# Kernel tuning notes

Measured on AMD Instinct MI355X. Metric: run time of the kernel, lower is better.

## Reference

```python
import jax, jax.numpy as jnp
import numpy as np

EMBED_DIM = 768
NUM_HEADS = 12
HEAD_DIM = EMBED_DIM // NUM_HEADS
SCALE = HEAD_DIM ** -0.5


def setup_inputs() -> dict:
    key = jax.random.key(0)
    k1, k2, k3, k4, k5 = jax.random.split(key, 5)
    B, T = 8, 1024
    init = 0.02
    return {
        "hidden_states": jax.random.normal(k1, (B, T, EMBED_DIM), dtype=jnp.float32),
        "qkv_w": jax.random.normal(k2, (EMBED_DIM, 3 * EMBED_DIM), dtype=jnp.float32) * init,
        "qkv_b": jnp.zeros((3 * EMBED_DIM,), dtype=jnp.float32),
        "proj_w": jax.random.normal(k3, (EMBED_DIM, EMBED_DIM), dtype=jnp.float32) * init,
        "proj_b": jnp.zeros((EMBED_DIM,), dtype=jnp.float32),
    }


def reference(hidden_states, qkv_w, qkv_b, proj_w, proj_b):
    B, T, E = hidden_states.shape
    # fused QKV projection: [B, T, 3E] -> [3, B, H, T, Dh]
    mixed = hidden_states @ qkv_w + qkv_b
    mixed = mixed.reshape(B, T, 3, NUM_HEADS, HEAD_DIM).transpose(2, 0, 3, 1, 4)
    q, k, v = mixed[0], mixed[1], mixed[2]
    # scores: [B, H, T, T]
    scores = jnp.einsum("bhqd,bhkd->bhqk", q, k) * SCALE
    probs = jax.nn.softmax(scores, axis=-1)
    # context: [B, T, H, Dh] -> [B, T, E]
    ctx = jnp.einsum("bhqk,bhkd->bqhd", probs, v).reshape(B, T, E)
    return ctx @ proj_w + proj_b
```

## Files before the change

kernel.cpp:

```cpp
#include <hip/hip_runtime.h>
#include <hip/hip_bf16.h>

#define B_ 8
#define T_ 1024
#define E_ 768
#define H_ 12
#define DH_ 64
#define E3_ 2304
#define M_ (B_ * T_)
#define SCALE_LOG2E 0.18033688011112042f

typedef __attribute__((ext_vector_type(8))) short short8;
typedef __attribute__((ext_vector_type(4))) float float4_;
typedef __attribute__((ext_vector_type(4))) unsigned short ushort4_;

__device__ __forceinline__ unsigned short f2bf(float f) {
    union { float f; unsigned int u; } v; v.f = f;
    unsigned int r = v.u + 0x7fffu + ((v.u >> 16) & 1u);
    return (unsigned short)(r >> 16);
}

__device__ __forceinline__ void gld_lds16(const unsigned short* g, unsigned short* l) {
    __builtin_amdgcn_global_load_lds(
        (const __attribute__((address_space(1))) void*)g,
        (__attribute__((address_space(3))) void*)l,
        16, 0, 0);
}

__global__ __launch_bounds__(256) void prep(const float* __restrict__ hs,
                                            const float* __restrict__ qkv_w,
                                            const float* __restrict__ proj_w,
                                            unsigned short* __restrict__ hs_bf,
                                            unsigned short* __restrict__ qkvwT,
                                            unsigned short* __restrict__ projwT) {
    __shared__ float tile[32][33];
    const int id = blockIdx.x;
    const int tid = threadIdx.x;
    if (id < 6144) {
        const int i = (id * 256 + tid) * 4;
        float4_ v = *(const float4_*)(hs + i);
        ushort4_ o;
        o.x = f2bf(v.x); o.y = f2bf(v.y); o.z = f2bf(v.z); o.w = f2bf(v.w);
        *(ushort4_*)(hs_bf + i) = o;
        return;
    }
    const float* W; unsigned short* Wt; int N, bx, by;
    if (id < 6144 + 1728) {
        const int t = id - 6144; W = qkv_w; Wt = qkvwT; N = E3_;
        bx = t % 72; by = t / 72;
    } else {
        const int t = id - 7872; W = proj_w; Wt = projwT; N = E_;
        bx = t % 24; by = t / 24;
    }
    const int k0 = by * 32, n0 = bx * 32;
    const int tx = tid & 31, ty = tid >> 5;
    for (int i = ty; i < 32; i += 8)
        tile[i][tx] = W[(size_t)(k0 + i) * N + n0 + tx];
    __syncthreads();
    for (int i = ty; i < 32; i += 8)
        Wt[(size_t)(n0 + i) * E_ + k0 + tx] = f2bf(tile[tx][i]);
}

template <int STORE_MODE>
__global__ __launch_bounds__(256) void gemm_mfma(const unsigned short* __restrict__ A,
                                                 const unsigned short* __restrict__ Wt,
                                                 const float* __restrict__ bias,
                                                 void* __restrict__ Cout,
                                                 unsigned short* __restrict__ Vt,
                                                 int M, int N, int K) {
    __shared__ __align__(16) unsigned short Al[2][128 * 32];
    __shared__ __align__(16) unsigned short Wl[2][128 * 32];

    const int tid = threadIdx.x;
    const int lane = tid & 63;
    const int w = tid >> 6;

    const int id = blockIdx.x;
    const int xcd = id & 7;
    const int slot = id >> 3;
    const int bx = slot >> 3;
    const int by = xcd * 8 + (slot & 7);
    const int bm = by * 128;
    const int bn = bx * 128;

    const int wm = (w >> 1) * 64;
    const int wn = (w & 1) * 64;
    const int quad = lane >> 4;
    const int l16 = lane & 15;

    const int srow = w * 32 + (lane >> 2);
    const int schunk = (lane & 3) * 8;
    const int sbase = w * 32 * 32 + lane * 8;

    const unsigned short* ga = A + (size_t)(bm + srow) * K + schunk;
    const unsigned short* gw = Wt + (size_t)(bn + srow) * K + schunk;

    float4_ acc[4][4] = {};

    gld_lds16(ga, &Al[0][sbase]);
    gld_lds16(ga + (size_t)16 * K, &Al[0][sbase + 512]);
    gld_lds16(gw, &Wl[0][sbase]);
    gld_lds16(gw + (size_t)16 * K, &Wl[0][sbase + 512]);

    const int NI = K >> 5;
    for (int i = 0; i < NI; ++i) {
        const int cur = i & 1;
        __syncthreads();
        if (i + 1 < NI) {
            const unsigned short* ga2 = ga + (size_t)(i + 1) * 32;
            const unsigned short* gw2 = gw + (size_t)(i + 1) * 32;
            const int nxt = cur ^ 1;
            gld_lds16(ga2, &Al[nxt][sbase]);
            gld_lds16(ga2 + (size_t)16 * K, &Al[nxt][sbase + 512]);
            gld_lds16(gw2, &Wl[nxt][sbase]);
            gld_lds16(gw2 + (size_t)16 * K, &Wl[nxt][sbase + 512]);
        }
        short8 af[4], bf[4];
#pragma unroll
        for (int mt = 0; mt < 4; ++mt)
            af[mt] = *(const short8*)(&Al[cur][(wm + mt * 16 + l16) * 32 + quad * 8]);
#pragma unroll
        for (int nt = 0; nt < 4; ++nt)
            bf[nt] = *(const short8*)(&Wl[cur][(wn + nt * 16 + l16) * 32 + quad * 8]);
#pragma unroll
        for (int mt = 0; mt < 4; ++mt)
#pragma unroll
            for (int nt = 0; nt < 4; ++nt)
                acc[mt][nt] = __builtin_amdgcn_mfma_f32_16x16x32_bf16(af[mt], bf[nt],
                                                                      acc[mt][nt], 0, 0, 0);
    }

    if (STORE_MODE == 2 && bn >= 1536) {
        const int b = bm >> 10;
        const int tloc = (bm & 1023) + wm;
#pragma unroll
        for (int nt = 0; nt < 4; ++nt) {
            const int col = bn + wn + nt * 16 + l16;
            const int n = col - 1536;
            const int h = n >> 6, d = n & 63;
            const float bv = bias[col];
            const size_t vrow = (size_t)((b * H_ + h) * 64 + d) * T_;
#pragma unroll
            for (int mt = 0; mt < 4; ++mt) {
                ushort4_ pk;
                pk.x = f2bf(acc[mt][nt][0] + bv);
                pk.y = f2bf(acc[mt][nt][1] + bv);
                pk.z = f2bf(acc[mt][nt][2] + bv);
                pk.w = f2bf(acc[mt][nt][3] + bv);
                *(ushort4_*)(Vt + vrow + tloc + mt * 16 + quad * 4) = pk;
            }
        }
    } else {
#pragma unroll
        for (int nt = 0; nt < 4; ++nt) {
            const int col = bn + wn + nt * 16 + l16;
            const float bv = bias[col];
#pragma unroll
            for (int mt = 0; mt < 4; ++mt) {
#pragma unroll
                for (int i = 0; i < 4; ++i) {
                    const int row = bm + wm + mt * 16 + quad * 4 + i;
                    const float v = acc[mt][nt][i] + bv;
                    if (STORE_MODE >= 1)
                        ((unsigned short*)Cout)[(size_t)row * N + col] = f2bf(v);
                    else
                        ((float*)Cout)[(size_t)row * N + col] = v;
                }
            }
        }
    }
}

__global__ __launch_bounds__(256) void attn_mfma(const unsigned short* __restrict__ mixed,
                                                 const unsigned short* __restrict__ Vt,
                                                 unsigned short* __restrict__ ctx) {
    const int bh = blockIdx.x;
    const int b = bh / H_;
    const int h = bh % H_;
    const int q0 = blockIdx.y * 128;
    const int tid = threadIdx.x;
    const int lane = tid & 63;
    const int w = tid >> 6;
    const int quad = lane >> 4;
    const int l16 = lane & 15;

    __shared__ __align__(16) unsigned short Kl[8 * 520];
    __shared__ __align__(16) unsigned short Vl[8 * 520];
    __shared__ __align__(16) unsigned short Pl[4][32 * 72];
    unsigned short* pw = &Pl[w][0];

    short8 qf[2][2];
#pragma unroll
    for (int hh = 0; hh < 2; ++hh) {
        const size_t qrow = (size_t)(b * T_ + q0 + w * 32 + hh * 16 + l16) * E3_ + h * 64;
        qf[hh][0] = *(const short8*)(mixed + qrow + quad * 8);
        qf[hh][1] = *(const short8*)(mixed + qrow + 32 + quad * 8);
    }

    float4_ o[2][4] = {};
    float4_ lp[2] = {};

    const size_t kbase = (size_t)(b * T_) * E3_ + E_ + h * 64;
    const size_t vtb = (size_t)bh * 64 * T_;

    const int srow = tid >> 3;
    const int sc = tid & 7;

    for (int kv0 = 0; kv0 < T_; kv0 += 64) {
        short8 k1 = *(const short8*)(mixed + kbase + (size_t)(kv0 + srow) * E3_ + sc * 8);
        short8 k2 = *(const short8*)(mixed + kbase + (size_t)(kv0 + srow + 32) * E3_ + sc * 8);
        short8 v1 = *(const short8*)(Vt + vtb + (size_t)srow * T_ + kv0 + sc * 8);
        short8 v2 = *(const short8*)(Vt + vtb + (size_t)(srow + 32) * T_ + kv0 + sc * 8);
        __syncthreads();
        *(short8*)(&Kl[sc * 520 + srow * 8]) = k1;
        *(short8*)(&Kl[sc * 520 + (srow + 32) * 8]) = k2;
        *(short8*)(&Vl[sc * 520 + srow * 8]) = v1;
        *(short8*)(&Vl[sc * 520 + (srow + 32) * 8]) = v2;
        __syncthreads();

        float4_ s[2][4];
#pragma unroll
        for (int nt = 0; nt < 4; ++nt) {
            const int key = nt * 16 + l16;
            short8 kf0 = *(const short8*)(&Kl[quad * 520 + key * 8]);
            short8 kf1 = *(const short8*)(&Kl[(4 + quad) * 520 + key * 8]);
#pragma unroll
            for (int hh = 0; hh < 2; ++hh) {
                float4_ z = {};
                z = __builtin_amdgcn_mfma_f32_16x16x32_bf16(qf[hh][0], kf0, z, 0, 0, 0);
                s[hh][nt] = __builtin_amdgcn_mfma_f32_16x16x32_bf16(qf[hh][1], kf1, z, 0, 0, 0);
            }
        }

#pragma unroll
        for (int hh = 0; hh < 2; ++hh) {
#pragma unroll
            for (int nt = 0; nt < 4; ++nt) {
#pragma unroll
                for (int i = 0; i < 4; ++i) {
                    const float p = exp2f(s[hh][nt][i] * SCALE_LOG2E);
                    lp[hh][i] += p;
                    pw[(hh * 16 + quad * 4 + i) * 72 + nt * 16 + l16] = f2bf(p);
                }
            }
        }

        short8 pf[2][2];
#pragma unroll
        for (int hh = 0; hh < 2; ++hh) {
            pf[hh][0] = *(const short8*)(&pw[(hh * 16 + l16) * 72 + quad * 8]);
            pf[hh][1] = *(const short8*)(&pw[(hh * 16 + l16) * 72 + 32 + quad * 8]);
        }

#pragma unroll
        for (int dt = 0; dt < 4; ++dt) {
            const int d = dt * 16 + l16;
            short8 vf0 = *(const short8*)(&Vl[quad * 520 + d * 8]);
            short8 vf1 = *(const short8*)(&Vl[(4 + quad) * 520 + d * 8]);
#pragma unroll
            for (int hh = 0; hh < 2; ++hh) {
                o[hh][dt] = __builtin_amdgcn_mfma_f32_16x16x32_bf16(pf[hh][0], vf0, o[hh][dt], 0, 0, 0);
                o[hh][dt] = __builtin_amdgcn_mfma_f32_16x16x32_bf16(pf[hh][1], vf1, o[hh][dt], 0, 0, 0);
            }
        }
    }

#pragma unroll
    for (int hh = 0; hh < 2; ++hh) {
        float4_ inv;
#pragma unroll
        for (int i = 0; i < 4; ++i) {
            float v = lp[hh][i];
#pragma unroll
            for (int msk = 1; msk < 16; msk <<= 1) v += __shfl_xor(v, msk, 64);
            inv[i] = 1.0f / v;
        }
#pragma unroll
        for (int dt = 0; dt < 4; ++dt) {
#pragma unroll
            for (int i = 0; i < 4; ++i) {
                const float v = o[hh][dt][i] * inv[i];
                const size_t row = (size_t)(b * T_ + q0 + w * 32 + hh * 16 + quad * 4 + i);
                ctx[row * E_ + h * 64 + dt * 16 + l16] = f2bf(v);
            }
        }
    }
}

extern "C" void kernel_launch(void* const* d_in, const int* in_sizes, int n_in,
                              void* d_out, int out_size, void* d_ws, size_t ws_size,
                              hipStream_t stream) {
    const float* hs     = (const float*)d_in[0];
    const float* qkv_w  = (const float*)d_in[1];
    const float* qkv_b  = (const float*)d_in[2];
    const float* proj_w = (const float*)d_in[3];
    const float* proj_b = (const float*)d_in[4];
    float* out = (float*)d_out;

    unsigned short* hs_bf  = (unsigned short*)d_ws;
    unsigned short* qkvwT  = hs_bf + (size_t)M_ * E_;
    unsigned short* projwT = qkvwT + (size_t)E3_ * E_;
    unsigned short* mixed  = projwT + (size_t)E_ * E_;
    unsigned short* Vt     = mixed + (size_t)M_ * E3_;
    unsigned short* ctx    = hs_bf;

    prep<<<8448, 256, 0, stream>>>(hs, qkv_w, proj_w, hs_bf, qkvwT, projwT);

    gemm_mfma<2><<<(E3_ / 128) * (M_ / 128), 256, 0, stream>>>(hs_bf, qkvwT, qkv_b,
                                                               (void*)mixed, Vt, M_, E3_, E_);
    attn_mfma<<<dim3(B_ * H_, T_ / 128), 256, 0, stream>>>(mixed, Vt, ctx);
    gemm_mfma<0><<<(E_ / 128) * (M_ / 128), 256, 0, stream>>>(ctx, projwT, proj_b,
                                                              (void*)out, nullptr, M_, E_, E_);
}
```

Baseline: 217.1 us.

## Compute transposed scores via swapped MFMA operands and fold scale into Q projection

Swaps the MFMA operands so each lane holds four consecutive keys for one query row. That lets P be written to LDS as one packed 8-byte store instead of four scalar 2-byte stores. The softmax scale times log2(e) is folded into the Q columns in the QKV GEMM epilogue, removing a multiply per score. Row sums become one scalar per lane, reduced with two shuffles instead of sixteen, which changes how the normalizer is gathered and adds a slight bf16 rounding change on Q.

```diff
diff --git a/kernel.cpp b/kernel.cpp
--- a/kernel.cpp
+++ b/kernel.cpp
@@ -151,6 +151,7 @@
             }
         }
     } else {
+        const float qs = (STORE_MODE == 2 && bn < 768) ? SCALE_LOG2E : 1.0f;
 #pragma unroll
         for (int nt = 0; nt < 4; ++nt) {
             const int col = bn + wn + nt * 16 + l16;
@@ -160,7 +161,7 @@
 #pragma unroll
                 for (int i = 0; i < 4; ++i) {
                     const int row = bm + wm + mt * 16 + quad * 4 + i;
-                    const float v = acc[mt][nt][i] + bv;
+                    const float v = (acc[mt][nt][i] + bv) * qs;
                     if (STORE_MODE >= 1)
                         ((unsigned short*)Cout)[(size_t)row * N + col] = f2bf(v);
                     else
@@ -198,7 +199,7 @@
     }
 
     float4_ o[2][4] = {};
-    float4_ lp[2] = {};
+    float lps[2] = {0.0f, 0.0f};
 
     const size_t kbase = (size_t)(b * T_) * E3_ + E_ + h * 64;
     const size_t vtb = (size_t)bh * 64 * T_;
@@ -218,7 +219,7 @@
         *(short8*)(&Vl[sc * 520 + (srow + 32) * 8]) = v2;
         __syncthreads();
 
-        float4_ s[2][4];
+        float4_ st[2][4];
 #pragma unroll
         for (int nt = 0; nt < 4; ++nt) {
             const int key = nt * 16 + l16;
@@ -227,8 +228,8 @@
 #pragma unroll
             for (int hh = 0; hh < 2; ++hh) {
                 float4_ z = {};
-                z = __builtin_amdgcn_mfma_f32_16x16x32_bf16(qf[hh][0], kf0, z, 0, 0, 0);
-                s[hh][nt] = __builtin_amdgcn_mfma_f32_16x16x32_bf16(qf[hh][1], kf1, z, 0, 0, 0);
+                z = __builtin_amdgcn_mfma_f32_16x16x32_bf16(kf0, qf[hh][0], z, 0, 0, 0);
+                st[hh][nt] = __builtin_amdgcn_mfma_f32_16x16x32_bf16(kf1, qf[hh][1], z, 0, 0, 0);
             }
         }
 
@@ -236,12 +237,14 @@
         for (int hh = 0; hh < 2; ++hh) {
 #pragma unroll
             for (int nt = 0; nt < 4; ++nt) {
-#pragma unroll
-                for (int i = 0; i < 4; ++i) {
-                    const float p = exp2f(s[hh][nt][i] * SCALE_LOG2E);
-                    lp[hh][i] += p;
-                    pw[(hh * 16 + quad * 4 + i) * 72 + nt * 16 + l16] = f2bf(p);
-                }
+                ushort4_ pk;
+                float p0 = exp2f(st[hh][nt][0]);
+                float p1 = exp2f(st[hh][nt][1]);
+                float p2 = exp2f(st[hh][nt][2]);
+                float p3 = exp2f(st[hh][nt][3]);
+                pk.x = f2bf(p0); pk.y = f2bf(p1); pk.z = f2bf(p2); pk.w = f2bf(p3);
+                lps[hh] += (p0 + p1) + (p2 + p3);
+                *(ushort4_*)(&pw[(hh * 16 + l16) * 72 + nt * 16 + quad * 4]) = pk;
             }
         }
 
@@ -267,14 +270,13 @@
 
 #pragma unroll
     for (int hh = 0; hh < 2; ++hh) {
+        float l = lps[hh];
+        l += __shfl_xor(l, 16, 64);
+        l += __shfl_xor(l, 32, 64);
         float4_ inv;
 #pragma unroll
-        for (int i = 0; i < 4; ++i) {
-            float v = lp[hh][i];
-#pragma unroll
-            for (int msk = 1; msk < 16; msk <<= 1) v += __shfl_xor(v, msk, 64);
-            inv[i] = 1.0f / v;
-        }
+        for (int i = 0; i < 4; ++i)
+            inv[i] = 1.0f / __shfl(l, quad * 4 + i, 16);
 #pragma unroll
         for (int dt = 0; dt < 4; ++dt) {
 #pragma unroll
```

Result: no change. 216.2 us (-0.4%).
